# Optimization experiments

Measured on AMD Instinct MI355X. Metric: run time of the kernel, lower is better.

The kernel has to match this reference:

```python
import jax, jax.numpy as jnp
import numpy as np

Z_DIM = 64
K = 2048
N = 32768


def setup_inputs() -> dict:
    key = jax.random.key(0)
    k1, k2 = jax.random.split(key)
    x = jax.random.normal(k1, (N, Z_DIM), dtype=jnp.float32)
    # init.normal_(locs, std=sqrt(z_dim))
    locs = jax.random.normal(k2, (K, Z_DIM), dtype=jnp.float32) * np.sqrt(Z_DIM)
    logits = jnp.zeros((K,), dtype=jnp.float32)  # maxent buffer
    return {"x": x, "locs": locs, "logits": logits}


def reference(x, locs, logits):
    d = x.shape[-1]
    var = jnp.float32(d)  # scale = sqrt(z_dim) -> variance = z_dim
    # squared distances [N, K] via cdist expansion (avoids [N,K,d] intermediate)
    sq = (
        jnp.sum(x * x, axis=-1, keepdims=True)
        + jnp.sum(locs * locs, axis=-1)[None, :]
        - 2.0 * (x @ locs.T)
    )
    # Independent Normal log prob summed over z_dim
    log_norm_const = d * (0.5 * jnp.log(2.0 * jnp.pi) + 0.5 * jnp.log(var))
    comp_log_prob = -0.5 * sq / var - log_norm_const  # [N, K]
    mix_logits = jax.nn.log_softmax(logits)  # Categorical normalizes logits
    wlp = comp_log_prob + mix_logits  # weighted_log_prob, [N, K]
    log_prob = jax.nn.logsumexp(wlp, axis=-1)  # [N]
    modes = jnp.argmax(wlp, axis=-1)  # assign_modes, [N]
    quantized = locs[modes]  # hard_quantize, [N, z_dim]
    return log_prob, quantized
```

## Files before the change

kernel.cpp:

```cpp
#include <hip/hip_runtime.h>
#include <math.h>

#define N_SAMP 32768
#define K_COMP 2048
#define ZD 64
#define LNC 191.896324792608546f
#define LN2F 0.69314718055994531f
#define INV_LN2 1.44269504088896340f
#define S2C 0.02254211001388974f

#define STAGES 16
#define STAGE_B 16384

typedef __attribute__((ext_vector_type(8))) short short8;
typedef __attribute__((ext_vector_type(4))) float v4f;

#if __has_builtin(__builtin_amdgcn_exp2f)
#define EXP2(x) __builtin_amdgcn_exp2f(x)
#else
#define EXP2(x) exp2f(x)
#endif

typedef const __attribute__((address_space(1))) unsigned int* gas_t;
typedef __attribute__((address_space(3))) unsigned int* las_t;
__device__ inline void gload_lds16(const void* g, void* l) {
    __builtin_amdgcn_global_load_lds((gas_t)g, (las_t)l, 16, 0, 0);
}

__device__ inline unsigned short f2bf(float f) {
    unsigned int u = __float_as_uint(f);
    u += 0x7fffu + ((u >> 16) & 1u);
    return (unsigned short)(u >> 16);
}
__device__ inline float bf2f(unsigned short h) {
    return __uint_as_float(((unsigned int)h) << 16);
}

__global__ __launch_bounds__(256) void prep_kernel(
    const float* __restrict__ locs, const float* __restrict__ logits,
    float* __restrict__ ck2, float* __restrict__ lse_out,
    char* __restrict__ lf) {
    if (blockIdx.x < 64) {
        int gid = blockIdx.x * 256 + threadIdx.x;
        int k = gid >> 3;
        int dc = gid & 7;
        int T = k >> 4, n = k & 15;

        const float* src = locs + (size_t)k * ZD + dc * 8;
        float4 u0 = *(const float4*)(src);
        float4 u1 = *(const float4*)(src + 4);
        float a[8] = {u0.x, u0.y, u0.z, u0.w, u1.x, u1.y, u1.z, u1.w};

        short8 h;
        float sq = 0.f;
#pragma unroll
        for (int j = 0; j < 8; ++j) {
            h[j] = (short)f2bf(a[j]);
            sq = fmaf(a[j], a[j], sq);
        }
        *(short8*)(lf + (size_t)T * 2048 + (dc >> 2) * 1024 +
                   ((size_t)(n + 16 * (dc & 3))) * 16) = h;

        sq += __shfl_xor(sq, 1);
        sq += __shfl_xor(sq, 2);
        sq += __shfl_xor(sq, 4);
        if (dc == 0) ck2[k] = (logits[k] - sq * (1.0f / 128.0f)) * INV_LN2;
    } else {
        __shared__ float red[4];
        int tid = threadIdx.x;
        int wv = tid >> 6, ln = tid & 63;
        float lm = -INFINITY;
        for (int i = tid; i < K_COMP; i += 256) lm = fmaxf(lm, logits[i]);
#pragma unroll
        for (int d = 1; d < 64; d <<= 1) lm = fmaxf(lm, __shfl_xor(lm, d));
        if (ln == 0) red[wv] = lm;
        __syncthreads();
        float M = fmaxf(fmaxf(red[0], red[1]), fmaxf(red[2], red[3]));
        float ls = 0.f;
        for (int i = tid; i < K_COMP; i += 256) ls += __expf(logits[i] - M);
#pragma unroll
        for (int d = 1; d < 64; d <<= 1) ls += __shfl_xor(ls, d);
        __syncthreads();
        if (ln == 0) red[wv] = ls;
        __syncthreads();
        if (tid == 0) *lse_out = M + __logf(red[0] + red[1] + red[2] + red[3]);
    }
}

__global__ __launch_bounds__(512, 4) void mix_kernel(
    const float* __restrict__ x, const float* __restrict__ locs,
    const char* __restrict__ lf, const float* __restrict__ ck2,
    const float* __restrict__ lse_ptr, float* __restrict__ out) {

    __shared__ char buf[2][STAGE_B];
    __shared__ float wm1[2][64], wm2[2][64], wm3[2][64], wsum[2][64];
    __shared__ int   wi1[2][64], wi2[2][64], wi3[2][64];
    __shared__ float xsq_sh[64];
    __shared__ int   cb[3][64];
    __shared__ int   amax_sh[64];

    const int tid  = threadIdx.x;
    const int lane = tid & 63;
    const int wv   = __builtin_amdgcn_readfirstlane(tid >> 6);
    const int sg   = __builtin_amdgcn_readfirstlane(wv & 3);
    const int kg   = __builtin_amdgcn_readfirstlane(wv >> 2);
    const int n    = lane & 15;
    const int quad = lane >> 4;
    const int sbase = blockIdx.x * 64;
    const int srow  = sbase + sg * 16 + n;

    short8 bh0, bh1, bl0, bl1;
    {
        const float* xp = x + (size_t)srow * ZD + quad * 8;
        float4 u0 = *(const float4*)(xp);
        float4 u1 = *(const float4*)(xp + 4);
        float4 u2 = *(const float4*)(xp + 32);
        float4 u3 = *(const float4*)(xp + 36);
        float a[8] = {u0.x, u0.y, u0.z, u0.w, u1.x, u1.y, u1.z, u1.w};
        float b[8] = {u2.x, u2.y, u2.z, u2.w, u3.x, u3.y, u3.z, u3.w};
        float p = 0.f;
#pragma unroll
        for (int j = 0; j < 8; ++j) {
            unsigned short h;
            h = f2bf(a[j]); bh0[j] = (short)h; bl0[j] = (short)f2bf(a[j] - bf2f(h));
            h = f2bf(b[j]); bh1[j] = (short)h; bl1[j] = (short)f2bf(b[j] - bf2f(h));
            p = fmaf(a[j], a[j], p);
            p = fmaf(b[j], b[j], p);
        }
        p += __shfl_xor(p, 16);
        p += __shfl_xor(p, 32);
        if (kg == 0 && quad == 0) xsq_sh[sg * 16 + n] = p;
    }

    const char* gsrc0 = lf + (size_t)((wv >> 2) * 64 + (wv & 3)) * 2048 + lane * 16;
    char* ldst0 = &buf[0][wv * 2048];

#define DMA(S, b) do {                                                   \
    const char* _g = gsrc0 + (size_t)(S) * (4 * 2048);                   \
    char* _l = ldst0 + (b) * STAGE_B;                                    \
    gload_lds16(_g, _l);                                                 \
    gload_lds16(_g + 1024, _l + 1024);                                   \
} while (0)

    float m1 = -1e30f, m2 = -1e30f, m3 = -1e30f;
    int i1 = 0, i2 = 0, i3 = 0;
    float s0 = 0.f, s1 = 0.f;

#define INS(v, kb) do {                                                  \
    bool c1 = (v) > m1, c2 = (v) > m2, c3 = (v) > m3;                    \
    m3 = c2 ? m2 : (c3 ? (v) : m3);  i3 = c2 ? i2 : (c3 ? (kb) : i3);    \
    m2 = c1 ? m1 : (c2 ? (v) : m2);  i2 = c1 ? i1 : (c2 ? (kb) : i2);    \
    m1 = c1 ? (v) : m1;              i1 = c1 ? (kb) : i1;                \
} while (0)

#define EPI(acc, cc, kb) do {                                            \
    float w0 = fmaf((acc).x, S2C, (cc).x);                               \
    float w1 = fmaf((acc).y, S2C, (cc).y);                               \
    float w2 = fmaf((acc).z, S2C, (cc).z);                               \
    float w3 = fmaf((acc).w, S2C, (cc).w);                               \
    s0 += EXP2(w0) + EXP2(w1);                                           \
    s1 += EXP2(w2) + EXP2(w3);                                           \
    float v4 = fmaxf(fmaxf(w0, w1), fmaxf(w2, w3));                      \
    INS(v4, kb);                                                         \
} while (0)

    DMA(0, 0);
    __syncthreads();

    for (int S = 0; S < STAGES; ++S) {
        const int b = S & 1;
        if (S + 1 < STAGES) DMA(S + 1, b ^ 1);

        const int tb = kg * 64 + 4 * S;
        const float* ckS = ck2 + tb * 16 + quad * 4;
        const char* base = &buf[b][(kg * 4) * 2048 + lane * 16];
        const int kb0 = tb * 16 + quad * 4;

#pragma unroll
        for (int jp = 0; jp < 4; jp += 2) {
            const char* p0 = base + jp * 2048;
            const char* p1 = p0 + 2048;
            short8 a00 = *(const short8*)(p0);
            short8 a01 = *(const short8*)(p0 + 1024);
            short8 a10 = *(const short8*)(p1);
            short8 a11 = *(const short8*)(p1 + 1024);
            float4 cc0 = *(const float4*)(ckS + jp * 16);
            float4 cc1 = *(const float4*)(ckS + jp * 16 + 16);

            v4f ca = {0.f, 0.f, 0.f, 0.f};
            v4f cb2_ = {0.f, 0.f, 0.f, 0.f};
            ca   = __builtin_amdgcn_mfma_f32_16x16x32_bf16(a00, bh0, ca, 0, 0, 0);
            cb2_ = __builtin_amdgcn_mfma_f32_16x16x32_bf16(a10, bh0, cb2_, 0, 0, 0);
            ca   = __builtin_amdgcn_mfma_f32_16x16x32_bf16(a01, bh1, ca, 0, 0, 0);
            cb2_ = __builtin_amdgcn_mfma_f32_16x16x32_bf16(a11, bh1, cb2_, 0, 0, 0);
            ca   = __builtin_amdgcn_mfma_f32_16x16x32_bf16(a00, bl0, ca, 0, 0, 0);
            cb2_ = __builtin_amdgcn_mfma_f32_16x16x32_bf16(a10, bl0, cb2_, 0, 0, 0);
            ca   = __builtin_amdgcn_mfma_f32_16x16x32_bf16(a01, bl1, ca, 0, 0, 0);
            cb2_ = __builtin_amdgcn_mfma_f32_16x16x32_bf16(a11, bl1, cb2_, 0, 0, 0);

            EPI(ca,   cc0, kb0 + jp * 16);
            EPI(cb2_, cc1, kb0 + jp * 16 + 16);
        }
        __syncthreads();
    }

    float sum = s0 + s1;
#pragma unroll
    for (int d = 16; d <= 32; d <<= 1) {
        sum += __shfl_xor(sum, d);
        float M1 = __shfl_xor(m1, d), M2 = __shfl_xor(m2, d), M3 = __shfl_xor(m3, d);
        int   I1 = __shfl_xor(i1, d), I2 = __shfl_xor(i2, d), I3 = __shfl_xor(i3, d);
        INS(M1, I1); INS(M2, I2); INS(M3, I3);
    }
    if (quad == 0) {
        int s = sg * 16 + n;
        wm1[kg][s] = m1; wm2[kg][s] = m2; wm3[kg][s] = m3;
        wi1[kg][s] = i1; wi2[kg][s] = i2; wi3[kg][s] = i3;
        wsum[kg][s] = sum;
    }
    __syncthreads();

    if (tid < 64) {
        float m1 = wm1[0][tid], m2 = wm2[0][tid], m3 = wm3[0][tid];
        int   i1 = wi1[0][tid], i2 = wi2[0][tid], i3 = wi3[0][tid];
        INS(wm1[1][tid], wi1[1][tid]);
        INS(wm2[1][tid], wi2[1][tid]);
        INS(wm3[1][tid], wi3[1][tid]);
        float S = wsum[0][tid] + wsum[1][tid];
        float bias = -xsq_sh[tid] * (1.0f / 128.0f) - LNC;
        out[sbase + tid] = fmaf(__log2f(S), LN2F, bias - lse_ptr[0]);
        cb[0][tid] = i1; cb[1][tid] = i2; cb[2][tid] = i3;
    }
    __syncthreads();

    {
        int s = tid >> 3;
        int j = tid & 7;
        const float4* xrow = (const float4*)(x + (size_t)(sbase + s) * ZD);
        float bestv = -1e30f;
        int bestk = 0x7fffffff;
#pragma unroll
        for (int ci = j; ci < 12; ci += 8) {
            int k = cb[ci >> 2][s] + (ci & 3);
            const float4* lrow = (const float4*)(locs + (size_t)k * ZD);
            float dot = 0.f;
#pragma unroll
            for (int dd = 0; dd < 16; ++dd) {
                float4 xv = xrow[dd];
                float4 lv = lrow[dd];
                dot = fmaf(xv.x, lv.x, dot);
                dot = fmaf(xv.y, lv.y, dot);
                dot = fmaf(xv.z, lv.z, dot);
                dot = fmaf(xv.w, lv.w, dot);
            }
            float v = fmaf(dot, S2C, ck2[k]);
            if (v > bestv || (v == bestv && k < bestk)) { bestv = v; bestk = k; }
        }
#pragma unroll
        for (int d = 1; d <= 4; d <<= 1) {
            float ov = __shfl_xor(bestv, d);
            int   ok = __shfl_xor(bestk, d);
            if (ov > bestv || (ov == bestv && ok < bestk)) { bestv = ov; bestk = ok; }
        }
        if (j == 0) amax_sh[s] = bestk;
    }
    __syncthreads();

    const float4* lq = (const float4*)locs;
    float4* oq = (float4*)(out + N_SAMP + (size_t)sbase * ZD);
#pragma unroll
    for (int i = tid; i < 64 * (ZD / 4); i += 512) {
        int r = i >> 4, c = i & 15;
        oq[i] = lq[(size_t)amax_sh[r] * (ZD / 4) + c];
    }
#undef DMA
#undef INS
#undef EPI
}

extern "C" void kernel_launch(void* const* d_in, const int* in_sizes, int n_in,
                              void* d_out, int out_size, void* d_ws, size_t ws_size,
                              hipStream_t stream) {
    const float* x      = (const float*)d_in[0];
    const float* locs   = (const float*)d_in[1];
    const float* logits = (const float*)d_in[2];
    float* out = (float*)d_out;

    float* ck2 = (float*)d_ws;
    float* lse = (float*)((char*)d_ws + 8192);
    char*  lf  = (char*)d_ws + 16384;

    prep_kernel<<<65, 256, 0, stream>>>(locs, logits, ck2, lse, lf);
    mix_kernel<<<N_SAMP / 64, 512, 0, stream>>>(x, locs, lf, ck2, lse, out);
}
```

Baseline: 106.0 us.

## Drop bf16 split-precision MFMA, load centroids from global into registers, halve block rows

Drops the low-half bf16 correction terms, so each dot product uses a single bf16 pass and needs half the MFMAs. Top-3 candidates are still rescored in fp32, which keeps the argmax exact. The LDS double-buffered DMA pipeline is replaced by direct register prefetch of centroid fragments from global/L2. Each block now covers 32 samples, with all 8 waves splitting K and reducing through shared memory, and the launch bound is raised to allow more resident blocks. The risks are lower log_prob accuracy from bf16-only distances and more global/L2 traffic for centroids, since each block reloads them.

Result: no change. 103.9 us (-1.9%).

```diff
diff --git a/kernel.cpp b/kernel.cpp
--- a/kernel.cpp
+++ b/kernel.cpp
@@ -9,9 +9,6 @@
 #define INV_LN2 1.44269504088896340f
 #define S2C 0.02254211001388974f
 
-#define STAGES 16
-#define STAGE_B 16384
-
 typedef __attribute__((ext_vector_type(8))) short short8;
 typedef __attribute__((ext_vector_type(4))) float v4f;
 
@@ -21,19 +18,10 @@
 #define EXP2(x) exp2f(x)
 #endif
 
-typedef const __attribute__((address_space(1))) unsigned int* gas_t;
-typedef __attribute__((address_space(3))) unsigned int* las_t;
-__device__ inline void gload_lds16(const void* g, void* l) {
-    __builtin_amdgcn_global_load_lds((gas_t)g, (las_t)l, 16, 0, 0);
-}
-
 __device__ inline unsigned short f2bf(float f) {
     unsigned int u = __float_as_uint(f);
     u += 0x7fffu + ((u >> 16) & 1u);
     return (unsigned short)(u >> 16);
-}
-__device__ inline float bf2f(unsigned short h) {
-    return __uint_as_float(((unsigned int)h) << 16);
 }
 
 __global__ __launch_bounds__(256) void prep_kernel(
@@ -87,153 +75,155 @@
     }
 }
 
-__global__ __launch_bounds__(512, 4) void mix_kernel(
+__global__ __launch_bounds__(512, 6) void mix_kernel(
     const float* __restrict__ x, const float* __restrict__ locs,
     const char* __restrict__ lf, const float* __restrict__ ck2,
     const float* __restrict__ lse_ptr, float* __restrict__ out) {
 
-    __shared__ char buf[2][STAGE_B];
-    __shared__ float wm1[2][64], wm2[2][64], wm3[2][64], wsum[2][64];
-    __shared__ int   wi1[2][64], wi2[2][64], wi3[2][64];
-    __shared__ float xsq_sh[64];
-    __shared__ int   cb[3][64];
-    __shared__ int   amax_sh[64];
+    __shared__ float pf[8][32][4];
+    __shared__ int   pi[8][32][4];
+    __shared__ float xsq_sh[32];
+    __shared__ int   cb[3][32];
+    __shared__ int   amax_sh[32];
 
     const int tid  = threadIdx.x;
     const int lane = tid & 63;
-    const int wv   = __builtin_amdgcn_readfirstlane(tid >> 6);
-    const int sg   = __builtin_amdgcn_readfirstlane(wv & 3);
-    const int kg   = __builtin_amdgcn_readfirstlane(wv >> 2);
+    const int kg   = __builtin_amdgcn_readfirstlane(tid >> 6);
     const int n    = lane & 15;
     const int quad = lane >> 4;
-    const int sbase = blockIdx.x * 64;
-    const int srow  = sbase + sg * 16 + n;
-
-    short8 bh0, bh1, bl0, bl1;
+    const int sbase = blockIdx.x * 32;
+
+    short8 bh0, bh1, bh2, bh3;
     {
-        const float* xp = x + (size_t)srow * ZD + quad * 8;
+        const float* xp = x + (size_t)(sbase + n) * ZD + quad * 8;
         float4 u0 = *(const float4*)(xp);
         float4 u1 = *(const float4*)(xp + 4);
         float4 u2 = *(const float4*)(xp + 32);
         float4 u3 = *(const float4*)(xp + 36);
+        const float* yp = x + (size_t)(sbase + 16 + n) * ZD + quad * 8;
+        float4 v0 = *(const float4*)(yp);
+        float4 v1 = *(const float4*)(yp + 4);
+        float4 v2 = *(const float4*)(yp + 32);
+        float4 v3 = *(const float4*)(yp + 36);
         float a[8] = {u0.x, u0.y, u0.z, u0.w, u1.x, u1.y, u1.z, u1.w};
         float b[8] = {u2.x, u2.y, u2.z, u2.w, u3.x, u3.y, u3.z, u3.w};
-        float p = 0.f;
+        float c[8] = {v0.x, v0.y, v0.z, v0.w, v1.x, v1.y, v1.z, v1.w};
+        float d[8] = {v2.x, v2.y, v2.z, v2.w, v3.x, v3.y, v3.z, v3.w};
+        float pA = 0.f, pB = 0.f;
 #pragma unroll
         for (int j = 0; j < 8; ++j) {
-            unsigned short h;
-            h = f2bf(a[j]); bh0[j] = (short)h; bl0[j] = (short)f2bf(a[j] - bf2f(h));
-            h = f2bf(b[j]); bh1[j] = (short)h; bl1[j] = (short)f2bf(b[j] - bf2f(h));
-            p = fmaf(a[j], a[j], p);
-            p = fmaf(b[j], b[j], p);
-        }
-        p += __shfl_xor(p, 16);
-        p += __shfl_xor(p, 32);
-        if (kg == 0 && quad == 0) xsq_sh[sg * 16 + n] = p;
-    }
-
-    const char* gsrc0 = lf + (size_t)((wv >> 2) * 64 + (wv & 3)) * 2048 + lane * 16;
-    char* ldst0 = &buf[0][wv * 2048];
-
-#define DMA(S, b) do {                                                   \
-    const char* _g = gsrc0 + (size_t)(S) * (4 * 2048);                   \
-    char* _l = ldst0 + (b) * STAGE_B;                                    \
-    gload_lds16(_g, _l);                                                 \
-    gload_lds16(_g + 1024, _l + 1024);                                   \
+            bh0[j] = (short)f2bf(a[j]);
+            bh1[j] = (short)f2bf(b[j]);
+            bh2[j] = (short)f2bf(c[j]);
+            bh3[j] = (short)f2bf(d[j]);
+            pA = fmaf(a[j], a[j], pA); pA = fmaf(b[j], b[j], pA);
+            pB = fmaf(c[j], c[j], pB); pB = fmaf(d[j], d[j], pB);
+        }
+        pA += __shfl_xor(pA, 16); pA += __shfl_xor(pA, 32);
+        pB += __shfl_xor(pB, 16); pB += __shfl_xor(pB, 32);
+        if (kg == 0) {
+            if (quad == 0) xsq_sh[n] = pA;
+            if (quad == 1) xsq_sh[16 + n] = pB;
+        }
+    }
+
+    const char* aw = lf + (size_t)(kg * 16) * 2048 + lane * 16;
+    const float* ckw = ck2 + kg * 256 + quad * 4;
+    const int kb0 = kg * 256 + quad * 4;
+
+    short8 fa[2][2];
+    float4 fc[2];
+
+#define LOADA(slot, t) do {                                              \
+    const char* _p = aw + (size_t)(t) * 2048;                            \
+    fa[slot][0] = *(const short8*)(_p);                                  \
+    fa[slot][1] = *(const short8*)(_p + 1024);                           \
+    fc[slot] = *(const float4*)(ckw + (t) * 16);                         \
 } while (0)
 
-    float m1 = -1e30f, m2 = -1e30f, m3 = -1e30f;
-    int i1 = 0, i2 = 0, i3 = 0;
-    float s0 = 0.f, s1 = 0.f;
-
-#define INS(v, kb) do {                                                  \
+    float sA = 0.f, m1A = -1e30f, m2A = -1e30f, m3A = -1e30f;
+    int i1A = 0, i2A = 0, i3A = 0;
+    float sB = 0.f, m1B = -1e30f, m2B = -1e30f, m3B = -1e30f;
+    int i1B = 0, i2B = 0, i3B = 0;
+
+#define INS(m1, m2, m3, i1, i2, i3, v, kb) do {                          \
     bool c1 = (v) > m1, c2 = (v) > m2, c3 = (v) > m3;                    \
     m3 = c2 ? m2 : (c3 ? (v) : m3);  i3 = c2 ? i2 : (c3 ? (kb) : i3);    \
     m2 = c1 ? m1 : (c2 ? (v) : m2);  i2 = c1 ? i1 : (c2 ? (kb) : i2);    \
     m1 = c1 ? (v) : m1;              i1 = c1 ? (kb) : i1;                \
 } while (0)
 
-#define EPI(acc, cc, kb) do {                                            \
+#define EPI(acc, cc, kb, S, M1, M2, M3, I1, I2, I3) do {                 \
     float w0 = fmaf((acc).x, S2C, (cc).x);                               \
     float w1 = fmaf((acc).y, S2C, (cc).y);                               \
     float w2 = fmaf((acc).z, S2C, (cc).z);                               \
     float w3 = fmaf((acc).w, S2C, (cc).w);                               \
-    s0 += EXP2(w0) + EXP2(w1);                                           \
-    s1 += EXP2(w2) + EXP2(w3);                                           \
+    S += (EXP2(w0) + EXP2(w1)) + (EXP2(w2) + EXP2(w3));                  \
     float v4 = fmaxf(fmaxf(w0, w1), fmaxf(w2, w3));                      \
-    INS(v4, kb);                                                         \
+    INS(M1, M2, M3, I1, I2, I3, v4, kb);                                 \
 } while (0)
 
-    DMA(0, 0);
+    LOADA(0, 0);
+#pragma unroll
+    for (int t = 0; t < 16; ++t) {
+        const int slot = t & 1;
+        if (t + 1 < 16) LOADA(slot ^ 1, t + 1);
+
+        v4f accA = {0.f, 0.f, 0.f, 0.f};
+        v4f accB = {0.f, 0.f, 0.f, 0.f};
+        accA = __builtin_amdgcn_mfma_f32_16x16x32_bf16(fa[slot][0], bh0, accA, 0, 0, 0);
+        accB = __builtin_amdgcn_mfma_f32_16x16x32_bf16(fa[slot][0], bh2, accB, 0, 0, 0);
+        accA = __builtin_amdgcn_mfma_f32_16x16x32_bf16(fa[slot][1], bh1, accA, 0, 0, 0);
+        accB = __builtin_amdgcn_mfma_f32_16x16x32_bf16(fa[slot][1], bh3, accB, 0, 0, 0);
+
+        const int kb = kb0 + t * 16;
+        float4 cc = fc[slot];
+        EPI(accA, cc, kb, sA, m1A, m2A, m3A, i1A, i2A, i3A);
+        EPI(accB, cc, kb, sB, m1B, m2B, m3B, i1B, i2B, i3B);
+    }
+
+#pragma unroll
+    for (int d = 16; d <= 32; d <<= 1) {
+        sA += __shfl_xor(sA, d);
+        sB += __shfl_xor(sB, d);
+        float M1, M2, M3; int I1, I2, I3;
+        M1 = __shfl_xor(m1A, d); M2 = __shfl_xor(m2A, d); M3 = __shfl_xor(m3A, d);
+        I1 = __shfl_xor(i1A, d); I2 = __shfl_xor(i2A, d); I3 = __shfl_xor(i3A, d);
+        INS(m1A, m2A, m3A, i1A, i2A, i3A, M1, I1);
+        INS(m1A, m2A, m3A, i1A, i2A, i3A, M2, I2);
+        INS(m1A, m2A, m3A, i1A, i2A, i3A, M3, I3);
+        M1 = __shfl_xor(m1B, d); M2 = __shfl_xor(m2B, d); M3 = __shfl_xor(m3B, d);
+        I1 = __shfl_xor(i1B, d); I2 = __shfl_xor(i2B, d); I3 = __shfl_xor(i3B, d);
+        INS(m1B, m2B, m3B, i1B, i2B, i3B, M1, I1);
+        INS(m1B, m2B, m3B, i1B, i2B, i3B, M2, I2);
+        INS(m1B, m2B, m3B, i1B, i2B, i3B, M3, I3);
+    }
+    if (quad == 0) {
+        pf[kg][n][0] = sA; pf[kg][n][1] = m1A; pf[kg][n][2] = m2A; pf[kg][n][3] = m3A;
+        pi[kg][n][0] = i1A; pi[kg][n][1] = i2A; pi[kg][n][2] = i3A;
+        pf[kg][16 + n][0] = sB; pf[kg][16 + n][1] = m1B;
+        pf[kg][16 + n][2] = m2B; pf[kg][16 + n][3] = m3B;
+        pi[kg][16 + n][0] = i1B; pi[kg][16 + n][1] = i2B; pi[kg][16 + n][2] = i3B;
+    }
     __syncthreads();
 
-    for (int S = 0; S < STAGES; ++S) {
-        const int b = S & 1;
-        if (S + 1 < STAGES) DMA(S + 1, b ^ 1);
-
-        const int tb = kg * 64 + 4 * S;
-        const float* ckS = ck2 + tb * 16 + quad * 4;
-        const char* base = &buf[b][(kg * 4) * 2048 + lane * 16];
-        const int kb0 = tb * 16 + quad * 4;
-
-#pragma unroll
-        for (int jp = 0; jp < 4; jp += 2) {
-            const char* p0 = base + jp * 2048;
-            const char* p1 = p0 + 2048;
-            short8 a00 = *(const short8*)(p0);
-            short8 a01 = *(const short8*)(p0 + 1024);
-            short8 a10 = *(const short8*)(p1);
-            short8 a11 = *(const short8*)(p1 + 1024);
-            float4 cc0 = *(const float4*)(ckS + jp * 16);
-            float4 cc1 = *(const float4*)(ckS + jp * 16 + 16);
-
-            v4f ca = {0.f, 0.f, 0.f, 0.f};
-            v4f cb2_ = {0.f, 0.f, 0.f, 0.f};
-            ca   = __builtin_amdgcn_mfma_f32_16x16x32_bf16(a00, bh0, ca, 0, 0, 0);
-            cb2_ = __builtin_amdgcn_mfma_f32_16x16x32_bf16(a10, bh0, cb2_, 0, 0, 0);
-            ca   = __builtin_amdgcn_mfma_f32_16x16x32_bf16(a01, bh1, ca, 0, 0, 0);
-            cb2_ = __builtin_amdgcn_mfma_f32_16x16x32_bf16(a11, bh1, cb2_, 0, 0, 0);
-            ca   = __builtin_amdgcn_mfma_f32_16x16x32_bf16(a00, bl0, ca, 0, 0, 0);
-            cb2_ = __builtin_amdgcn_mfma_f32_16x16x32_bf16(a10, bl0, cb2_, 0, 0, 0);
-            ca   = __builtin_amdgcn_mfma_f32_16x16x32_bf16(a01, bl1, ca, 0, 0, 0);
-            cb2_ = __builtin_amdgcn_mfma_f32_16x16x32_bf16(a11, bl1, cb2_, 0, 0, 0);
-
-            EPI(ca,   cc0, kb0 + jp * 16);
-            EPI(cb2_, cc1, kb0 + jp * 16 + 16);
-        }
-        __syncthreads();
-    }
-
-    float sum = s0 + s1;
-#pragma unroll
-    for (int d = 16; d <= 32; d <<= 1) {
-        sum += __shfl_xor(sum, d);
-        float M1 = __shfl_xor(m1, d), M2 = __shfl_xor(m2, d), M3 = __shfl_xor(m3, d);
-        int   I1 = __shfl_xor(i1, d), I2 = __shfl_xor(i2, d), I3 = __shfl_xor(i3, d);
-        INS(M1, I1); INS(M2, I2); INS(M3, I3);
-    }
-    if (quad == 0) {
-        int s = sg * 16 + n;
-        wm1[kg][s] = m1; wm2[kg][s] = m2; wm3[kg][s] = m3;
-        wi1[kg][s] = i1; wi2[kg][s] = i2; wi3[kg][s] = i3;
-        wsum[kg][s] = sum;
-    }
-    __syncthreads();
-
-    if (tid < 64) {
-        float m1 = wm1[0][tid], m2 = wm2[0][tid], m3 = wm3[0][tid];
-        int   i1 = wi1[0][tid], i2 = wi2[0][tid], i3 = wi3[0][tid];
-        INS(wm1[1][tid], wi1[1][tid]);
-        INS(wm2[1][tid], wi2[1][tid]);
-        INS(wm3[1][tid], wi3[1][tid]);
-        float S = wsum[0][tid] + wsum[1][tid];
+    if (tid < 32) {
+        float S = 0.f, m1 = -1e30f, m2 = -1e30f, m3 = -1e30f;
+        int i1 = 0, i2 = 0, i3 = 0;
+#pragma unroll
+        for (int g = 0; g < 8; ++g) {
+            S += pf[g][tid][0];
+            INS(m1, m2, m3, i1, i2, i3, pf[g][tid][1], pi[g][tid][0]);
+            INS(m1, m2, m3, i1, i2, i3, pf[g][tid][2], pi[g][tid][1]);
+            INS(m1, m2, m3, i1, i2, i3, pf[g][tid][3], pi[g][tid][2]);
+        }
         float bias = -xsq_sh[tid] * (1.0f / 128.0f) - LNC;
         out[sbase + tid] = fmaf(__log2f(S), LN2F, bias - lse_ptr[0]);
         cb[0][tid] = i1; cb[1][tid] = i2; cb[2][tid] = i3;
     }
     __syncthreads();
 
-    {
+    if (tid < 256) {
         int s = tid >> 3;
         int j = tid & 7;
         const float4* xrow = (const float4*)(x + (size_t)(sbase + s) * ZD);
@@ -266,14 +256,13 @@
     }
     __syncthreads();
 
-    const float4* lq = (const float4*)locs;
-    float4* oq = (float4*)(out + N_SAMP + (size_t)sbase * ZD);
-#pragma unroll
-    for (int i = tid; i < 64 * (ZD / 4); i += 512) {
-        int r = i >> 4, c = i & 15;
-        oq[i] = lq[(size_t)amax_sh[r] * (ZD / 4) + c];
-    }
-#undef DMA
+    {
+        const float4* lq = (const float4*)locs;
+        float4* oq = (float4*)(out + N_SAMP + (size_t)sbase * ZD);
+        int r = tid >> 4, c = tid & 15;
+        oq[tid] = lq[(size_t)amax_sh[r] * (ZD / 4) + c];
+    }
+#undef LOADA
 #undef INS
 #undef EPI
 }
@@ -291,5 +280,5 @@
     char*  lf  = (char*)d_ws + 16384;
 
     prep_kernel<<<65, 256, 0, stream>>>(locs, logits, ck2, lse, lf);
-    mix_kernel<<<N_SAMP / 64, 512, 0, stream>>>(x, locs, lf, ck2, lse, out);
-}
+    mix_kernel<<<N_SAMP / 32, 512, 0, stream>>>(x, locs, lf, ck2, lse, out);
+}
```
